# Performance work log

Measured on AMD Instinct MI355X. Metric: run time of the kernel, lower is better.

Reference implementation:

```python
import jax, jax.numpy as jnp
import numpy as np

CE_W = 2.0
LOV_W = 6.0
IGNORE_INDEX = 0  # CrossEntropyLoss(ignore_index=0); lovasz uses ignore=None


def _sem_loss(outputs, targets):
    P, C = outputs.shape
    log_p = jax.nn.log_softmax(outputs, axis=1)  # [P, C]

    # ---- cross entropy with ignore_index=0 (mean over valid) ----
    valid = targets != IGNORE_INDEX
    nll = -jnp.take_along_axis(log_p, targets[:, None], axis=1)[:, 0]  # [P]
    n_valid = jnp.maximum(valid.sum(), 1)
    ce = jnp.sum(jnp.where(valid, nll, 0.0)) / n_valid.astype(nll.dtype)

    # ---- lovasz-softmax over softmax probs, classes='present', ignore=None ----
    probas = jnp.exp(log_p)  # softmax(outputs, dim=1)
    # fg[c, p] = (targets[p] == c)
    fg = (targets[None, :] == jnp.arange(C)[:, None]).astype(probas.dtype)  # [C, P]
    errors = jnp.abs(fg - probas.T)  # [C, P]
    # sort errors descending per class; gather fg with same permutation
    perm = jnp.argsort(-errors, axis=1)  # [C, P]
    errors_sorted = jnp.take_along_axis(errors, perm, axis=1)
    fg_sorted = jnp.take_along_axis(fg, perm, axis=1)
    # lovasz_grad per class
    gts = fg_sorted.sum(axis=1, keepdims=True)  # [C, 1]
    intersection = gts - jnp.cumsum(fg_sorted, axis=1)
    union = gts + jnp.cumsum(1.0 - fg_sorted, axis=1)
    jac = 1.0 - intersection / union  # [C, P]
    grad = jnp.concatenate([jac[:, :1], jac[:, 1:] - jac[:, :-1]], axis=1)
    per_class_loss = jnp.sum(errors_sorted * grad, axis=1)  # [C]
    present = (gts[:, 0] > 0).astype(per_class_loss.dtype)  # classes='present' mask
    lov = jnp.sum(per_class_loss * present) / jnp.maximum(present.sum(), 1.0)

    return jnp.stack([CE_W * ce, LOV_W * lov])  # [sem_ce, sem_lov]


def setup_inputs() -> dict:
    key = jax.random.key(0)
    k1, k2 = jax.random.split(key)
    P, C = 2_000_000, 20
    outputs = jax.random.normal(k1, (P, C), dtype=jnp.float32)
    targets = jax.random.randint(k2, (P,), 0, C, dtype=jnp.int64)
    return {"outputs": outputs, "targets": targets}


def reference(outputs, targets):
    return _sem_loss(outputs, targets)
```

## Files before the change

### kernel.cpp

```cpp
#include <hip/hip_runtime.h>
#include <stdint.h>

typedef unsigned int u32;
typedef unsigned short u16;
typedef unsigned long long u64;

#define NB 512
#define NC 20
#define K1_BLOCK 256
#define HIST_U32 (NC * NB * 2)
#define DUMP_BYTES (HIST_U32 * 2)
#define OFF_CE   (HIST_U32 * 4)
#define OFF_CNT  (OFF_CE + 4)
#define OFF_DUMPS 98304
#define RESERVED  OFF_DUMPS

__global__ __launch_bounds__(K1_BLOCK) void k1_hist(
    const float* __restrict__ logits, const int* __restrict__ tgt, int P,
    u16* __restrict__ dumps, float* __restrict__ ce_sum, u32* __restrict__ valid_cnt)
{
    __shared__ u32 lds[HIST_U32];
    __shared__ float ce_w[4];
    __shared__ u32   cnt_w[4];

    for (int i = threadIdx.x; i < HIST_U32; i += K1_BLOCK) lds[i] = 0;
    __syncthreads();

    float ce_part = 0.f;
    u32   cnt_part = 0;

    for (long long idx = (long long)blockIdx.x * K1_BLOCK + threadIdx.x; idx < P;
         idx += (long long)gridDim.x * K1_BLOCK) {
        const float* row = logits + idx * NC;
        float4 v0 = *(const float4*)(row + 0);
        float4 v1 = *(const float4*)(row + 4);
        float4 v2 = *(const float4*)(row + 8);
        float4 v3 = *(const float4*)(row + 12);
        float4 v4 = *(const float4*)(row + 16);
        float x[NC] = { v0.x, v0.y, v0.z, v0.w,  v1.x, v1.y, v1.z, v1.w,
                        v2.x, v2.y, v2.z, v2.w,  v3.x, v3.y, v3.z, v3.w,
                        v4.x, v4.y, v4.z, v4.w };
        int t = tgt[idx];

        float mx = x[0];
        #pragma unroll
        for (int c = 1; c < NC; ++c) mx = fmaxf(mx, x[c]);

        float e[NC];
        float s = 0.f;
        #pragma unroll
        for (int c = 0; c < NC; ++c) { e[c] = __expf(x[c] - mx); s += e[c]; }
        float inv = 1.0f / s;
        float lse = __logf(s);

        float xt = 0.f;
        #pragma unroll
        for (int c = 0; c < NC; ++c) xt = (c == t) ? x[c] : xt;
        if (t != 0) { ce_part += (mx + lse - xt); cnt_part++; }

        #pragma unroll
        for (int c = 0; c < NC; ++c) {
            float p = e[c] * inv;
            float err = (c == t) ? (1.0f - p) : p;
            int b = (int)(err * (float)NB);
            b = b < 0 ? 0 : (b > NB - 1 ? NB - 1 : b);
            atomicAdd(&lds[c * NB + b], 1u);
            if (c == t) atomicAdd(&lds[NC * NB + c * NB + b], 1u);
        }
    }

    #pragma unroll
    for (int off = 32; off > 0; off >>= 1) {
        ce_part  += __shfl_down(ce_part, off);
        cnt_part += __shfl_down(cnt_part, off);
    }
    int lane = threadIdx.x & 63, wid = threadIdx.x >> 6;
    if (lane == 0) { ce_w[wid] = ce_part; cnt_w[wid] = cnt_part; }
    __syncthreads();
    if (threadIdx.x == 0) {
        atomicAdd(ce_sum,  ce_w[0] + ce_w[1] + ce_w[2] + ce_w[3]);
        atomicAdd(valid_cnt, cnt_w[0] + cnt_w[1] + cnt_w[2] + cnt_w[3]);
    }
    __syncthreads();

    u16* d = dumps + (size_t)blockIdx.x * HIST_U32;
    for (int i = threadIdx.x; i < HIST_U32; i += K1_BLOCK) d[i] = (u16)lds[i];
}

__global__ __launch_bounds__(256) void k2a_reduce(
    const u16* __restrict__ dumps, u32* __restrict__ final_hist, int nblk, int chunk)
{
    int counter = (blockIdx.x % 80) * 256 + threadIdx.x;
    int part    = blockIdx.x / 80;
    int b0 = part * chunk;
    int b1 = b0 + chunk; if (b1 > nblk) b1 = nblk;
    u32 ssum = 0;
    for (int blk = b0; blk < b1; ++blk)
        ssum += dumps[(size_t)blk * HIST_U32 + counter];
    if (ssum) atomicAdd(&final_hist[counter], ssum);
}

__device__ __forceinline__ float jac_of(float gts, u32 cf, u32 ct)
{
    float I = gts - (float)cf;
    float U = gts + (float)ct - (float)cf;
    return 1.0f - I / U;
}

__global__ __launch_bounds__(256) void k2b_final(
    const u32* __restrict__ final_hist, const float* __restrict__ ce_sum,
    const u32* __restrict__ valid_cnt, float* __restrict__ outp)
{
    __shared__ u64 sc[256];
    __shared__ float red[256];
    int t = threadIdx.x;

    float lovsum = 0.f;
    int prescnt = 0;

    for (int c = 0; c < NC; ++c) {
        int b0 = NB - 1 - (2 * t);
        int b1 = NB - 1 - (2 * t + 1);
        u32 t0 = final_hist[c * NB + b0], f0 = final_hist[NC * NB + c * NB + b0];
        u32 t1 = final_hist[c * NB + b1], f1 = final_hist[NC * NB + c * NB + b1];
        u64 v0 = ((u64)f0 << 32) | (u64)t0;
        u64 v1 = ((u64)f1 << 32) | (u64)t1;
        u64 local = v0 + v1;

        sc[t] = local;
        __syncthreads();
        for (int off = 1; off < 256; off <<= 1) {
            u64 add = (t >= off) ? sc[t - off] : 0ull;
            __syncthreads();
            sc[t] += add;
            __syncthreads();
        }
        u64 incl  = sc[t];
        u64 total = sc[255];
        float gts = (float)(u32)(total >> 32);

        float contrib = 0.f;
        if (gts > 0.f) {
            u64 excl = incl - local;
            u64 i0 = excl + v0;
            u64 i1 = i0 + v1;
            u32 cfE = (u32)(excl >> 32), ctE = (u32)excl;
            u32 cf0 = (u32)(i0 >> 32),   ct0 = (u32)i0;
            u32 cf1 = (u32)(i1 >> 32),   ct1 = (u32)i1;
            float jE = jac_of(gts, cfE, ctE);
            float j0 = jac_of(gts, cf0, ct0);
            float j1 = jac_of(gts, cf1, ct1);
            float e0 = ((float)b0 + 0.5f) * (1.0f / (float)NB);
            float e1 = ((float)b1 + 0.5f) * (1.0f / (float)NB);
            contrib = e0 * (j0 - jE) + e1 * (j1 - j0);
        }

        red[t] = contrib;
        __syncthreads();
        #pragma unroll
        for (int off = 128; off > 0; off >>= 1) {
            if (t < off) red[t] += red[t + off];
            __syncthreads();
        }
        if (t == 0 && gts > 0.f) { lovsum += red[0]; prescnt++; }
        __syncthreads();
    }

    if (t == 0) {
        u32 vc = *valid_cnt; if (vc < 1u) vc = 1u;
        float ce = *ce_sum / (float)vc;
        int pc = prescnt < 1 ? 1 : prescnt;
        float lov = lovsum / (float)pc;
        outp[0] = 2.0f * ce;
        outp[1] = 6.0f * lov;
    }
}

extern "C" void kernel_launch(void* const* d_in, const int* in_sizes, int n_in,
                              void* d_out, int out_size, void* d_ws, size_t ws_size,
                              hipStream_t stream)
{
    const float* logits = (const float*)d_in[0];
    const int*   tgt    = (const int*)d_in[1];
    int P = in_sizes[1];

    char* ws = (char*)d_ws;
    u32*  final_hist = (u32*)ws;
    float* ce_sum    = (float*)(ws + OFF_CE);
    u32*  valid_cnt  = (u32*)(ws + OFF_CNT);
    u16*  dumps      = (u16*)(ws + OFF_DUMPS);

    int nblk = 512;
    size_t avail = ws_size > (size_t)RESERVED ? ws_size - RESERVED : 0;
    int maxblk = (int)(avail / DUMP_BYTES);
    if (maxblk < 1) maxblk = 1;
    if (nblk > maxblk) nblk = maxblk;

    hipMemsetAsync(d_ws, 0, RESERVED, stream);
    hipLaunchKernelGGL(k1_hist, dim3(nblk), dim3(K1_BLOCK), 0, stream,
                       logits, tgt, P, dumps, ce_sum, valid_cnt);
    int split = nblk >= 8 ? 8 : 1;
    int chunk = (nblk + split - 1) / split;
    hipLaunchKernelGGL(k2a_reduce, dim3(80 * split), dim3(256), 0, stream,
                       dumps, final_hist, nblk, chunk);
    hipLaunchKernelGGL(k2b_final, dim3(1), dim3(256), 0, stream,
                       final_hist, ce_sum, valid_cnt, (float*)d_out);
}
```

Baseline: 117.1 us.

## Pack fg and total counts into one LDS counter and shrink histogram bins

Halves the histogram bins from 512 to 256 and packs the foreground and total counts into the high and low 16-bit halves of a single u32 LDS counter. This removes the separate foreground atomic and cuts per-block LDS from 80KB to 20KB, which allows more resident blocks per CU. The first kernel now uses 1024 blocks with launch bounds, and each wave issues its own global atomics for the cross-entropy sum and count. The reduction kernel unpacks the two halves, and the final kernel scans one bin per thread. The price is coarser bins, which makes the Lovasz approximation less accurate, and per-block counts must stay below 65536. The grid-stride loop also hardcodes the block count, so results would be wrong if the workspace cap lowers nblk.

```diff
diff --git a/kernel.cpp b/kernel.cpp
--- a/kernel.cpp
+++ b/kernel.cpp
@@ -5,32 +5,33 @@
 typedef unsigned short u16;
 typedef unsigned long long u64;
 
-#define NB 512
+#define NB 256
 #define NC 20
 #define K1_BLOCK 256
-#define HIST_U32 (NC * NB * 2)
-#define DUMP_BYTES (HIST_U32 * 2)
-#define OFF_CE   (HIST_U32 * 4)
+#define NCTR (NC * NB)
+#define DUMP_BYTES (NCTR * 4)
+#define FINAL_U32 (NCTR * 2)
+#define OFF_CE   (FINAL_U32 * 4)
 #define OFF_CNT  (OFF_CE + 4)
-#define OFF_DUMPS 98304
+#define OFF_DUMPS 65536
 #define RESERVED  OFF_DUMPS
-
-__global__ __launch_bounds__(K1_BLOCK) void k1_hist(
+#define NBLK_K1  1024
+
+__global__ __launch_bounds__(K1_BLOCK, 4) void k1_hist(
     const float* __restrict__ logits, const int* __restrict__ tgt, int P,
-    u16* __restrict__ dumps, float* __restrict__ ce_sum, u32* __restrict__ valid_cnt)
-{
-    __shared__ u32 lds[HIST_U32];
-    __shared__ float ce_w[4];
-    __shared__ u32   cnt_w[4];
-
-    for (int i = threadIdx.x; i < HIST_U32; i += K1_BLOCK) lds[i] = 0;
+    u32* __restrict__ dumps, float* __restrict__ ce_sum, u32* __restrict__ valid_cnt)
+{
+    __shared__ u32 lds[NCTR];
+
+    #pragma unroll
+    for (int i = threadIdx.x; i < NCTR; i += K1_BLOCK) lds[i] = 0;
     __syncthreads();
 
     float ce_part = 0.f;
     u32   cnt_part = 0;
 
     for (long long idx = (long long)blockIdx.x * K1_BLOCK + threadIdx.x; idx < P;
-         idx += (long long)gridDim.x * K1_BLOCK) {
+         idx += (long long)NBLK_K1 * K1_BLOCK) {
         const float* row = logits + idx * NC;
         float4 v0 = *(const float4*)(row + 0);
         float4 v1 = *(const float4*)(row + 4);
@@ -61,11 +62,11 @@
         #pragma unroll
         for (int c = 0; c < NC; ++c) {
             float p = e[c] * inv;
-            float err = (c == t) ? (1.0f - p) : p;
+            bool is_t = (c == t);
+            float err = is_t ? (1.0f - p) : p;
             int b = (int)(err * (float)NB);
-            b = b < 0 ? 0 : (b > NB - 1 ? NB - 1 : b);
-            atomicAdd(&lds[c * NB + b], 1u);
-            if (c == t) atomicAdd(&lds[NC * NB + c * NB + b], 1u);
+            b = b > NB - 1 ? NB - 1 : (b < 0 ? 0 : b);
+            atomicAdd(&lds[c * NB + b], is_t ? 0x10001u : 1u);
         }
     }
 
@@ -74,30 +75,32 @@
         ce_part  += __shfl_down(ce_part, off);
         cnt_part += __shfl_down(cnt_part, off);
     }
-    int lane = threadIdx.x & 63, wid = threadIdx.x >> 6;
-    if (lane == 0) { ce_w[wid] = ce_part; cnt_w[wid] = cnt_part; }
+    if ((threadIdx.x & 63) == 0) {
+        atomicAdd(ce_sum, ce_part);
+        atomicAdd(valid_cnt, cnt_part);
+    }
     __syncthreads();
-    if (threadIdx.x == 0) {
-        atomicAdd(ce_sum,  ce_w[0] + ce_w[1] + ce_w[2] + ce_w[3]);
-        atomicAdd(valid_cnt, cnt_w[0] + cnt_w[1] + cnt_w[2] + cnt_w[3]);
-    }
-    __syncthreads();
-
-    u16* d = dumps + (size_t)blockIdx.x * HIST_U32;
-    for (int i = threadIdx.x; i < HIST_U32; i += K1_BLOCK) d[i] = (u16)lds[i];
+
+    u32* d = dumps + (size_t)blockIdx.x * NCTR;
+    #pragma unroll
+    for (int i = threadIdx.x; i < NCTR; i += K1_BLOCK) d[i] = lds[i];
 }
 
 __global__ __launch_bounds__(256) void k2a_reduce(
-    const u16* __restrict__ dumps, u32* __restrict__ final_hist, int nblk, int chunk)
-{
-    int counter = (blockIdx.x % 80) * 256 + threadIdx.x;
-    int part    = blockIdx.x / 80;
+    const u32* __restrict__ dumps, u32* __restrict__ final_hist, int nblk, int chunk)
+{
+    int counter = (blockIdx.x % 20) * 256 + threadIdx.x;
+    int part    = blockIdx.x / 20;
     int b0 = part * chunk;
     int b1 = b0 + chunk; if (b1 > nblk) b1 = nblk;
-    u32 ssum = 0;
-    for (int blk = b0; blk < b1; ++blk)
-        ssum += dumps[(size_t)blk * HIST_U32 + counter];
-    if (ssum) atomicAdd(&final_hist[counter], ssum);
+    u32 lo = 0, hi = 0;
+    for (int blk = b0; blk < b1; ++blk) {
+        u32 v = dumps[(size_t)blk * NCTR + counter];
+        lo += v & 0xFFFFu;
+        hi += v >> 16;
+    }
+    if (lo) atomicAdd(&final_hist[counter], lo);
+    if (hi) atomicAdd(&final_hist[NCTR + counter], hi);
 }
 
 __device__ __forceinline__ float jac_of(float gts, u32 cf, u32 ct)
@@ -111,54 +114,44 @@
     const u32* __restrict__ final_hist, const float* __restrict__ ce_sum,
     const u32* __restrict__ valid_cnt, float* __restrict__ outp)
 {
-    __shared__ u64 sc[256];
-    __shared__ float red[256];
+    __shared__ u64 sc[NB];
+    __shared__ float red[NB];
     int t = threadIdx.x;
 
     float lovsum = 0.f;
     int prescnt = 0;
 
     for (int c = 0; c < NC; ++c) {
-        int b0 = NB - 1 - (2 * t);
-        int b1 = NB - 1 - (2 * t + 1);
-        u32 t0 = final_hist[c * NB + b0], f0 = final_hist[NC * NB + c * NB + b0];
-        u32 t1 = final_hist[c * NB + b1], f1 = final_hist[NC * NB + c * NB + b1];
-        u64 v0 = ((u64)f0 << 32) | (u64)t0;
-        u64 v1 = ((u64)f1 << 32) | (u64)t1;
-        u64 local = v0 + v1;
-
-        sc[t] = local;
+        int b = NB - 1 - t;
+        u32 tot = final_hist[c * NB + b];
+        u32 fg  = final_hist[NCTR + c * NB + b];
+        u64 v = ((u64)fg << 32) | (u64)tot;
+
+        sc[t] = v;
         __syncthreads();
-        for (int off = 1; off < 256; off <<= 1) {
+        for (int off = 1; off < NB; off <<= 1) {
             u64 add = (t >= off) ? sc[t - off] : 0ull;
             __syncthreads();
             sc[t] += add;
             __syncthreads();
         }
         u64 incl  = sc[t];
-        u64 total = sc[255];
+        u64 total = sc[NB - 1];
         float gts = (float)(u32)(total >> 32);
 
         float contrib = 0.f;
         if (gts > 0.f) {
-            u64 excl = incl - local;
-            u64 i0 = excl + v0;
-            u64 i1 = i0 + v1;
-            u32 cfE = (u32)(excl >> 32), ctE = (u32)excl;
-            u32 cf0 = (u32)(i0 >> 32),   ct0 = (u32)i0;
-            u32 cf1 = (u32)(i1 >> 32),   ct1 = (u32)i1;
-            float jE = jac_of(gts, cfE, ctE);
-            float j0 = jac_of(gts, cf0, ct0);
-            float j1 = jac_of(gts, cf1, ct1);
-            float e0 = ((float)b0 + 0.5f) * (1.0f / (float)NB);
-            float e1 = ((float)b1 + 0.5f) * (1.0f / (float)NB);
-            contrib = e0 * (j0 - jE) + e1 * (j1 - j0);
+            u64 excl = incl - v;
+            float jE = jac_of(gts, (u32)(excl >> 32), (u32)excl);
+            float jI = jac_of(gts, (u32)(incl >> 32), (u32)incl);
+            float eb = ((float)b + 0.5f) * (1.0f / (float)NB);
+            contrib = eb * (jI - jE);
         }
 
         red[t] = contrib;
         __syncthreads();
         #pragma unroll
-        for (int off = 128; off > 0; off >>= 1) {
+        for (int off = NB / 2; off > 0; off >>= 1) {
             if (t < off) red[t] += red[t + off];
             __syncthreads();
         }
@@ -188,9 +181,9 @@
     u32*  final_hist = (u32*)ws;
     float* ce_sum    = (float*)(ws + OFF_CE);
     u32*  valid_cnt  = (u32*)(ws + OFF_CNT);
-    u16*  dumps      = (u16*)(ws + OFF_DUMPS);
-
-    int nblk = 512;
+    u32*  dumps      = (u32*)(ws + OFF_DUMPS);
+
+    int nblk = NBLK_K1;
     size_t avail = ws_size > (size_t)RESERVED ? ws_size - RESERVED : 0;
     int maxblk = (int)(avail / DUMP_BYTES);
     if (maxblk < 1) maxblk = 1;
@@ -199,10 +192,10 @@
     hipMemsetAsync(d_ws, 0, RESERVED, stream);
     hipLaunchKernelGGL(k1_hist, dim3(nblk), dim3(K1_BLOCK), 0, stream,
                        logits, tgt, P, dumps, ce_sum, valid_cnt);
-    int split = nblk >= 8 ? 8 : 1;
+    int split = nblk >= 16 ? 16 : 1;
     int chunk = (nblk + split - 1) / split;
-    hipLaunchKernelGGL(k2a_reduce, dim3(80 * split), dim3(256), 0, stream,
+    hipLaunchKernelGGL(k2a_reduce, dim3(20 * split), dim3(256), 0, stream,
                        dumps, final_hist, nblk, chunk);
-    hipLaunchKernelGGL(k2b_final, dim3(1), dim3(256), 0, stream,
+    hipLaunchKernelGGL(k2b_final, dim3(1), dim3(NB), 0, stream,
                        final_hist, ce_sum, valid_cnt, (float*)d_out);
 }
```

Result: slower. 175.7 us (+50.1%).
